# Optimization experiments

Hardware: AMD Instinct MI355X
Metric: run time of the kernel (lower is better)

## Reference

```python
import jax, jax.numpy as jnp
import numpy as np

N_ROUTING = 3


def squash(s):
    # squash factor ||s|| / (1 + ||s||^2), applied per output capsule vector
    n = jnp.linalg.norm(s, axis=-1, keepdims=True)
    return n / (1.0 + n * n) * s


def setup_inputs() -> dict:
    key = jax.random.key(0)
    k1, k2 = jax.random.split(key)
    B, Ni, Di = 64, 2048, 8
    No, Do = 32, 16
    x = jax.random.normal(k1, (B, Ni, Di), dtype=jnp.float32)
    W = jax.random.normal(k2, (Ni, No, Do, Di), dtype=jnp.float32) * 0.05
    return {"x": x, "W": W}


def reference(x, W):
    # x: (B, Ni, Di); W: (Ni, No, Do, Di)
    # Per-capsule transform: x_hat[b,i,j,:] = W[i,j] @ x[b,i]
    x_hat = jnp.einsum('bni,nodi->bnod', x, W)          # (B, Ni, No, Do)
    x_hat_sg = jax.lax.stop_gradient(x_hat)
    B, Ni, No, Do = x_hat.shape
    b = jnp.zeros((B, Ni, No), dtype=x_hat.dtype)       # routing logits
    v = None
    for it in range(N_ROUTING):
        c = jax.nn.softmax(b, axis=2)                   # coupling over output caps
        if it == N_ROUTING - 1:
            s = jnp.einsum('bno,bnod->bod', c, x_hat)   # grads flow on last iter
            v = squash(s)
        else:
            s = jnp.einsum('bno,bnod->bod', c, x_hat_sg)
            v = squash(s)
            b = b + jnp.einsum('bod,bnod->bno', v, x_hat_sg)  # agreement update
    return v  # (B, No, Do)
```

## Files before the change

### kernel.cpp

```cpp
#include <hip/hip_runtime.h>
#include <hip/hip_bf16.h>
#include <math.h>

namespace {
constexpr int kB  = 64;
constexpr int kNi = 2048;
constexpr int kNo = 32;
constexpr int kDo = 16;
constexpr int kSeg   = kNo * kDo;
constexpr int kSlabs = 256;
constexpr int kNPer  = kNi / kSlabs;
}

typedef __attribute__((ext_vector_type(4)))  short s4;
typedef __attribute__((ext_vector_type(16))) float f16v;

__device__ __forceinline__ f16v mfma_32x32x8_bf16(s4 a, s4 b, f16v c) {
#if __has_builtin(__builtin_amdgcn_mfma_f32_32x32x8bf16_1k)
    return __builtin_amdgcn_mfma_f32_32x32x8bf16_1k(a, b, c, 0, 0, 0);
#else
    asm("v_mfma_f32_32x32x8_bf16 %0, %1, %2, %0" : "+v"(c) : "v"(a), "v"(b));
    return c;
#endif
}

__device__ __forceinline__ unsigned pack_bf16(float lo, float hi) {
    union { __hip_bfloat162 h; unsigned u; } v;
    v.h = __float22bfloat162_rn(make_float2(lo, hi));
    return v.u;
}
__device__ __forceinline__ float bf_lo(unsigned u) { return __uint_as_float(u << 16); }
__device__ __forceinline__ float bf_hi(unsigned u) { return __uint_as_float(u & 0xffff0000u); }

union A2 { int2 i; s4 s; };

__global__ __launch_bounds__(256, 4)
void caps_prep(const float* __restrict__ xg, const float* __restrict__ Wg,
               unsigned* __restrict__ wPack2, unsigned* __restrict__ xPack)
{
    const int t = blockIdx.x * 256 + threadIdx.x;
    const int nW = kNi * 16 * 64;
    if (t < nW) {
        const int n = t >> 10, rem = t & 1023, mt = rem >> 6, l = rem & 63;
        const float4 w = *reinterpret_cast<const float4*>(
            Wg + ((size_t)n * kSeg + mt * 32 + (l & 31)) * 8 + 4 * (l >> 5));
        const size_t base = (((size_t)n * 8 + (mt >> 1)) * 64 + l) * 4 + (mt & 1) * 2;
        uint2 u; u.x = pack_bf16(w.x, w.y); u.y = pack_bf16(w.z, w.w);
        *reinterpret_cast<uint2*>(wPack2 + base) = u;
    } else {
        const int t2 = t - nW;
        const int n = t2 >> 7, rem = t2 & 127, nt = rem >> 6, l = rem & 63;
        const float4 v = *reinterpret_cast<const float4*>(
            xg + ((size_t)(nt * 32 + (l & 31)) * kNi + n) * 8 + 4 * (l >> 5));
        uint2 u; u.x = pack_bf16(v.x, v.y); u.y = pack_bf16(v.z, v.w);
        *reinterpret_cast<uint2*>(xPack + (size_t)t2 * 2) = u;
    }
}


__global__ __launch_bounds__(512, 2)
void caps_acc0(const unsigned* __restrict__ wPack2, const unsigned* __restrict__ xPack,
               __hip_bfloat16* __restrict__ partial)
{
    const int tid = threadIdx.x;
    const int blk = blockIdx.x & (kSlabs - 1);
    const int nt  = blockIdx.x >> 8;
    const int w   = __builtin_amdgcn_readfirstlane(tid >> 6);
    const int l   = tid & 63;
    const int b   = nt * 32 + (l & 31);
    const int hi  = l >> 5;

    f16v acc0, acc1;
#pragma unroll
    for (int r = 0; r < 16; ++r) { acc0[r] = 0.0f; acc1[r] = 0.0f; }

    const int4* wp4 = reinterpret_cast<const int4*>(wPack2);
    const int2* xp2 = reinterpret_cast<const int2*>(xPack);
    const size_t abase = ((size_t)blk * 64 + w) * 64 + l;
    const size_t xbase = ((size_t)blk * 16 + nt) * 64 + l;

#pragma unroll 2
    for (int nn = 0; nn < kNPer; ++nn) {
        const int4 aw = wp4[abase + (size_t)nn * 512];
        const int2 bx = xp2[xbase + (size_t)nn * 128];
        A2 ua0; ua0.i = make_int2(aw.x, aw.y);
        A2 ua1; ua1.i = make_int2(aw.z, aw.w);
        A2 ub;  ub.i  = bx;
        acc0 = mfma_32x32x8_bf16(ua0.s, ub.s, acc0);
        acc1 = mfma_32x32x8_bf16(ua1.s, ub.s, acc1);
    }

#pragma unroll
    for (int m = 0; m < 2; ++m) {
        const int mt = 2 * w + m;
        const f16v& a = (m == 0) ? acc0 : acc1;
#pragma unroll
        for (int q = 0; q < 4; ++q) {
            const int od = mt * 32 + 8 * q + 4 * hi;
            uint2 u;
            u.x = pack_bf16(a[4 * q + 0], a[4 * q + 1]);
            u.y = pack_bf16(a[4 * q + 2], a[4 * q + 3]);
            *reinterpret_cast<uint2*>(
                partial + ((size_t)blk * kB + b) * kSeg + od) = u;
        }
    }
}

__global__ __launch_bounds__(512, 2)
void caps_routef(const unsigned* __restrict__ wPack2, const unsigned* __restrict__ xPack,
                 const float* __restrict__ vsumPack, __hip_bfloat16* __restrict__ partial)
{
    __shared__ float Zl[2][8][4][32];
    __shared__ unsigned cl[kNPer][16][32];

    const int tid = threadIdx.x;
    const int blk = blockIdx.x & (kSlabs - 1);
    const int nt  = blockIdx.x >> 8;
    const int w   = __builtin_amdgcn_readfirstlane(tid >> 6);
    const int l   = tid & 63;
    const int b32 = l & 31;
    const int b   = nt * 32 + b32;
    const int hi  = l >> 5;

    const int4* wp4 = reinterpret_cast<const int4*>(wPack2);
    const int2* xp2 = reinterpret_cast<const int2*>(xPack);
    const size_t abase = ((size_t)blk * 64 + w) * 64 + l;
    const size_t xbase = ((size_t)blk * 16 + nt) * 64 + l;

    {
        float vsp[2][16];
#pragma unroll
        for (int m = 0; m < 2; ++m) {
            const int mt = 2 * w + m;
            const float4* vp = reinterpret_cast<const float4*>(
                vsumPack + (((size_t)mt * 2 + hi) * 64 + b) * 16);
#pragma unroll
            for (int k = 0; k < 4; ++k) {
                const float4 v = vp[k];
                vsp[m][4 * k + 0] = v.x; vsp[m][4 * k + 1] = v.y;
                vsp[m][4 * k + 2] = v.z; vsp[m][4 * k + 3] = v.w;
            }
        }

        for (int h = 0; h < 2; ++h) {
            float e[4][4];
#pragma unroll
            for (int k = 0; k < 4; ++k) {
                const int nn = h * 4 + k;
                const int4 aw = wp4[abase + (size_t)nn * 512];
                const int2 bx = xp2[xbase + (size_t)nn * 128];
                A2 ua0; ua0.i = make_int2(aw.x, aw.y);
                A2 ua1; ua1.i = make_int2(aw.z, aw.w);
                A2 ub;  ub.i  = bx;
                f16v t0, t1;
#pragma unroll
                for (int r = 0; r < 16; ++r) { t0[r] = 0.0f; t1[r] = 0.0f; }
                t0 = mfma_32x32x8_bf16(ua0.s, ub.s, t0);
                t1 = mfma_32x32x8_bf16(ua1.s, ub.s, t1);
                {
                    float a0_ = fmaf(vsp[0][1], t0[1], vsp[0][0] * t0[0]);
                    float a1_ = fmaf(vsp[0][3], t0[3], vsp[0][2] * t0[2]);
                    float a2_ = fmaf(vsp[0][5], t0[5], vsp[0][4] * t0[4]);
                    float a3_ = fmaf(vsp[0][7], t0[7], vsp[0][6] * t0[6]);
                    float p0 = (a0_ + a1_) + (a2_ + a3_);
                    float b0_ = fmaf(vsp[0][9],  t0[9],  vsp[0][8]  * t0[8]);
                    float b1_ = fmaf(vsp[0][11], t0[11], vsp[0][10] * t0[10]);
                    float b2_ = fmaf(vsp[0][13], t0[13], vsp[0][12] * t0[12]);
                    float b3_ = fmaf(vsp[0][15], t0[15], vsp[0][14] * t0[14]);
                    float p1 = (b0_ + b1_) + (b2_ + b3_);
                    p0 += __shfl_xor(p0, 32);
                    p1 += __shfl_xor(p1, 32);
                    e[k][0] = exp2f(p0); e[k][1] = exp2f(p1);
                }
                {
                    float a0_ = fmaf(vsp[1][1], t1[1], vsp[1][0] * t1[0]);
                    float a1_ = fmaf(vsp[1][3], t1[3], vsp[1][2] * t1[2]);
                    float a2_ = fmaf(vsp[1][5], t1[5], vsp[1][4] * t1[4]);
                    float a3_ = fmaf(vsp[1][7], t1[7], vsp[1][6] * t1[6]);
                    float p0 = (a0_ + a1_) + (a2_ + a3_);
                    float b0_ = fmaf(vsp[1][9],  t1[9],  vsp[1][8]  * t1[8]);
                    float b1_ = fmaf(vsp[1][11], t1[11], vsp[1][10] * t1[10]);
                    float b2_ = fmaf(vsp[1][13], t1[13], vsp[1][12] * t1[12]);
                    float b3_ = fmaf(vsp[1][15], t1[15], vsp[1][14] * t1[14]);
                    float p1 = (b0_ + b1_) + (b2_ + b3_);
                    p0 += __shfl_xor(p0, 32);
                    p1 += __shfl_xor(p1, 32);
                    e[k][2] = exp2f(p0); e[k][3] = exp2f(p1);
                }
                if (l < 32)
                    Zl[h][w][k][l] = (e[k][0] + e[k][1]) + (e[k][2] + e[k][3]);
            }
            __syncthreads();
#pragma unroll
            for (int k = 0; k < 4; ++k) {
                float Z = 0.0f;
#pragma unroll
                for (int w2 = 0; w2 < 8; ++w2) Z += Zl[h][w2][k][b32];
                const float rz = __builtin_amdgcn_rcpf(Z);
                if (l < 32) {
                    cl[h * 4 + k][2 * w + 0][l] = pack_bf16(e[k][0] * rz, e[k][1] * rz);
                    cl[h * 4 + k][2 * w + 1][l] = pack_bf16(e[k][2] * rz, e[k][3] * rz);
                }
            }
        }
    }
    __syncthreads();
    __builtin_amdgcn_sched_barrier(0);

    float sacc[2][16];
#pragma unroll
    for (int r = 0; r < 16; ++r) { sacc[0][r] = 0.0f; sacc[1][r] = 0.0f; }

#pragma unroll 2
    for (int nn = 0; nn < kNPer; ++nn) {
        const int4 aw = wp4[abase + (size_t)nn * 512];
        const int2 bx = xp2[xbase + (size_t)nn * 128];
        A2 ua0; ua0.i = make_int2(aw.x, aw.y);
        A2 ua1; ua1.i = make_int2(aw.z, aw.w);
        A2 ub;  ub.i  = bx;
        const unsigned cp0 = cl[nn][2 * w + 0][b32];
        const unsigned cp1 = cl[nn][2 * w + 1][b32];
        f16v t0, t1;
#pragma unroll
        for (int r = 0; r < 16; ++r) { t0[r] = 0.0f; t1[r] = 0.0f; }
        t0 = mfma_32x32x8_bf16(ua0.s, ub.s, t0);
        t1 = mfma_32x32x8_bf16(ua1.s, ub.s, t1);
        const float c00 = bf_lo(cp0), c01 = bf_hi(cp0);
        const float c10 = bf_lo(cp1), c11 = bf_hi(cp1);
#pragma unroll
        for (int r = 0; r < 8; ++r) {
            sacc[0][r]     = fmaf(c00, t0[r],     sacc[0][r]);
            sacc[0][8 + r] = fmaf(c01, t0[8 + r], sacc[0][8 + r]);
            sacc[1][r]     = fmaf(c10, t1[r],     sacc[1][r]);
            sacc[1][8 + r] = fmaf(c11, t1[8 + r], sacc[1][8 + r]);
        }
    }

#pragma unroll
    for (int m = 0; m < 2; ++m) {
        const int mt = 2 * w + m;
#pragma unroll
        for (int q = 0; q < 4; ++q) {
            const int od = mt * 32 + 8 * q + 4 * hi;
            uint2 u;
            u.x = pack_bf16(sacc[m][4 * q + 0], sacc[m][4 * q + 1]);
            u.y = pack_bf16(sacc[m][4 * q + 2], sacc[m][4 * q + 3]);
            *reinterpret_cast<uint2*>(
                partial + ((size_t)blk * kB + b) * kSeg + od) = u;
        }
    }
}

template<int PASS>
__global__ __launch_bounds__(512, 2)
void caps_finish(const __hip_bfloat16* __restrict__ partial,
                 float* __restrict__ vsum, float* __restrict__ vsumPack,
                 float* __restrict__ out)
{
    const int b  = blockIdx.x >> 2;
    const int q  = blockIdx.x & 3;
    const int t  = threadIdx.x;
    const int tl = t & 127;
    const int cg = t >> 7;
    const int od = q * 128 + tl;

    const __hip_bfloat16* p = partial
        + ((size_t)(cg * 64) * kB + b) * kSeg + od;
    float s = 0.0f;
#pragma unroll 16
    for (int k = 0; k < 64; ++k)
        s += __bfloat162float(p[(size_t)k * (kB * kSeg)]);

    __shared__ float red[4][128];
    __shared__ float sq[128];
    __shared__ float fo[8];
    red[cg][tl] = s;
    __syncthreads();
    if (t < 128) {
        s = (red[0][tl] + red[1][tl]) + (red[2][tl] + red[3][tl]);
        if (PASS == 0) s *= (1.0f / 32.0f);
        sq[tl] = s * s;
    }
    __syncthreads();
    if (t < 8) {
        float n2 = 0.0f;
#pragma unroll
        for (int d = 0; d < 16; ++d) n2 += sq[t * 16 + d];
        fo[t] = sqrtf(n2) / (1.0f + n2);
    }
    __syncthreads();
    if (t < 128) {
        const float v = fo[tl >> 4] * s;
        float nv = v;
        if (PASS == 0) {
            vsum[(size_t)b * kSeg + od] = v;
        } else if (PASS == 1) {
            nv = vsum[(size_t)b * kSeg + od] + v;
            vsum[(size_t)b * kSeg + od] = nv;
        } else {
            out[(size_t)b * kSeg + od] = v;
        }
        if (PASS < 2) {
            const int mt = od >> 5, r5 = od & 31;
            const int hi = (r5 >> 2) & 1, reg = (r5 & 3) | ((r5 >> 3) << 2);
            vsumPack[(((size_t)mt * 2 + hi) * 64 + b) * 16 + reg] =
                nv * 1.44269504f;
        }
    }
}

extern "C" void kernel_launch(void* const* d_in, const int* in_sizes, int n_in,
                              void* d_out, int out_size, void* d_ws, size_t ws_size,
                              hipStream_t stream)
{
    const float* x = (const float*)d_in[0];
    const float* W = (const float*)d_in[1];
    float* out = (float*)d_out;

    char* base = (char*)d_ws;
    __hip_bfloat16* partial = (__hip_bfloat16*)base;
    base += (size_t)kSlabs * kB * kSeg * sizeof(__hip_bfloat16);
    float* vsum = (float*)base;
    base += (size_t)kB * kSeg * sizeof(float);
    float* vsumPack = (float*)base;
    base += (size_t)16 * 2 * 64 * 16 * sizeof(float);
    unsigned* wPack2 = (unsigned*)base;
    base += (size_t)kNi * 16 * 64 * 2 * sizeof(unsigned);
    unsigned* xPack = (unsigned*)base;

    caps_prep<<<dim3(9216), dim3(256), 0, stream>>>(x, W, wPack2, xPack);

    const dim3 gr(kSlabs * 2), br(512);
    const dim3 gf(kB * 4), bf(512);

    caps_acc0<<<gr, br, 0, stream>>>(wPack2, xPack, partial);
    caps_finish<0><<<gf, bf, 0, stream>>>(partial, vsum, vsumPack, out);
    caps_routef<<<gr, br, 0, stream>>>(wPack2, xPack, vsumPack, partial);
    caps_finish<1><<<gf, bf, 0, stream>>>(partial, vsum, vsumPack, out);
    caps_routef<<<gr, br, 0, stream>>>(wPack2, xPack, vsumPack, partial);
    caps_finish<2><<<gf, bf, 0, stream>>>(partial, vsum, vsumPack, out);
}
```

Before: 79.41 us.

## Fuse bf16 packing into first accumulation pass and vectorize finish reduction

The separate prep kernel is removed. The first routing accumulation kernel now reads fp32 W and x directly, packs them to bf16 and writes the packed buffers for later passes while also consuming them for its MFMA accumulation. Each block now covers both batch tiles, which halves the grid to 256 blocks, and each W load feeds four MFMAs. The finish kernel reads four bf16 values per load over 16 slab groups and reduces them through a larger shared array. This saves one launch and a round trip of the packed data, at the cost of fewer blocks in the fused kernel and more per-thread work.

```diff
diff --git a/kernel.cpp b/kernel.cpp
--- a/kernel.cpp
+++ b/kernel.cpp
@@ -34,74 +34,75 @@
 
 union A2 { int2 i; s4 s; };
 
-__global__ __launch_bounds__(256, 4)
-void caps_prep(const float* __restrict__ xg, const float* __restrict__ Wg,
-               unsigned* __restrict__ wPack2, unsigned* __restrict__ xPack)
-{
-    const int t = blockIdx.x * 256 + threadIdx.x;
-    const int nW = kNi * 16 * 64;
-    if (t < nW) {
-        const int n = t >> 10, rem = t & 1023, mt = rem >> 6, l = rem & 63;
-        const float4 w = *reinterpret_cast<const float4*>(
-            Wg + ((size_t)n * kSeg + mt * 32 + (l & 31)) * 8 + 4 * (l >> 5));
-        const size_t base = (((size_t)n * 8 + (mt >> 1)) * 64 + l) * 4 + (mt & 1) * 2;
-        uint2 u; u.x = pack_bf16(w.x, w.y); u.y = pack_bf16(w.z, w.w);
-        *reinterpret_cast<uint2*>(wPack2 + base) = u;
-    } else {
-        const int t2 = t - nW;
-        const int n = t2 >> 7, rem = t2 & 127, nt = rem >> 6, l = rem & 63;
-        const float4 v = *reinterpret_cast<const float4*>(
-            xg + ((size_t)(nt * 32 + (l & 31)) * kNi + n) * 8 + 4 * (l >> 5));
-        uint2 u; u.x = pack_bf16(v.x, v.y); u.y = pack_bf16(v.z, v.w);
-        *reinterpret_cast<uint2*>(xPack + (size_t)t2 * 2) = u;
-    }
-}
-
 
 __global__ __launch_bounds__(512, 2)
-void caps_acc0(const unsigned* __restrict__ wPack2, const unsigned* __restrict__ xPack,
-               __hip_bfloat16* __restrict__ partial)
+void caps_prepacc(const float* __restrict__ xg, const float* __restrict__ Wg,
+                  unsigned* __restrict__ wPack2, unsigned* __restrict__ xPack,
+                  __hip_bfloat16* __restrict__ partial)
 {
     const int tid = threadIdx.x;
-    const int blk = blockIdx.x & (kSlabs - 1);
-    const int nt  = blockIdx.x >> 8;
+    const int blk = blockIdx.x;
     const int w   = __builtin_amdgcn_readfirstlane(tid >> 6);
     const int l   = tid & 63;
-    const int b   = nt * 32 + (l & 31);
+    const int o32 = l & 31;
     const int hi  = l >> 5;
 
-    f16v acc0, acc1;
-#pragma unroll
-    for (int r = 0; r < 16; ++r) { acc0[r] = 0.0f; acc1[r] = 0.0f; }
-
-    const int4* wp4 = reinterpret_cast<const int4*>(wPack2);
-    const int2* xp2 = reinterpret_cast<const int2*>(xPack);
-    const size_t abase = ((size_t)blk * 64 + w) * 64 + l;
-    const size_t xbase = ((size_t)blk * 16 + nt) * 64 + l;
+    const float4* Wg4 = reinterpret_cast<const float4*>(Wg);
+    const float4* xg4 = reinterpret_cast<const float4*>(xg);
+
+    f16v acc00, acc01, acc10, acc11;
+#pragma unroll
+    for (int r = 0; r < 16; ++r) {
+        acc00[r] = 0.0f; acc01[r] = 0.0f; acc10[r] = 0.0f; acc11[r] = 0.0f;
+    }
 
 #pragma unroll 2
     for (int nn = 0; nn < kNPer; ++nn) {
-        const int4 aw = wp4[abase + (size_t)nn * 512];
-        const int2 bx = xp2[xbase + (size_t)nn * 128];
-        A2 ua0; ua0.i = make_int2(aw.x, aw.y);
-        A2 ua1; ua1.i = make_int2(aw.z, aw.w);
-        A2 ub;  ub.i  = bx;
-        acc0 = mfma_32x32x8_bf16(ua0.s, ub.s, acc0);
-        acc1 = mfma_32x32x8_bf16(ua1.s, ub.s, acc1);
-    }
-
-#pragma unroll
-    for (int m = 0; m < 2; ++m) {
-        const int mt = 2 * w + m;
-        const f16v& a = (m == 0) ? acc0 : acc1;
-#pragma unroll
-        for (int q = 0; q < 4; ++q) {
-            const int od = mt * 32 + 8 * q + 4 * hi;
-            uint2 u;
-            u.x = pack_bf16(a[4 * q + 0], a[4 * q + 1]);
-            u.y = pack_bf16(a[4 * q + 2], a[4 * q + 3]);
-            *reinterpret_cast<uint2*>(
-                partial + ((size_t)blk * kB + b) * kSeg + od) = u;
+        const int n = blk * kNPer + nn;
+        const float4 w0 = Wg4[((size_t)n * 512 + (2 * w + 0) * 32 + o32) * 2 + hi];
+        const float4 w1 = Wg4[((size_t)n * 512 + (2 * w + 1) * 32 + o32) * 2 + hi];
+        int4 wp;
+        wp.x = (int)pack_bf16(w0.x, w0.y);
+        wp.y = (int)pack_bf16(w0.z, w0.w);
+        wp.z = (int)pack_bf16(w1.x, w1.y);
+        wp.w = (int)pack_bf16(w1.z, w1.w);
+        reinterpret_cast<int4*>(wPack2)[((size_t)n * 8 + w) * 64 + l] = wp;
+
+        const float4 x0 = xg4[((size_t)(0 * 32 + o32) * kNi + n) * 2 + hi];
+        const float4 x1 = xg4[((size_t)(32 + o32) * kNi + n) * 2 + hi];
+        uint2 q0, q1;
+        q0.x = pack_bf16(x0.x, x0.y); q0.y = pack_bf16(x0.z, x0.w);
+        q1.x = pack_bf16(x1.x, x1.y); q1.y = pack_bf16(x1.z, x1.w);
+        *reinterpret_cast<uint2*>(xPack + ((size_t)(n * 2 + 0) * 64 + l) * 2) = q0;
+        *reinterpret_cast<uint2*>(xPack + ((size_t)(n * 2 + 1) * 64 + l) * 2) = q1;
+
+        A2 a0; a0.i = make_int2(wp.x, wp.y);
+        A2 a1; a1.i = make_int2(wp.z, wp.w);
+        A2 b0; b0.i = make_int2((int)q0.x, (int)q0.y);
+        A2 b1; b1.i = make_int2((int)q1.x, (int)q1.y);
+        acc00 = mfma_32x32x8_bf16(a0.s, b0.s, acc00);
+        acc01 = mfma_32x32x8_bf16(a1.s, b0.s, acc01);
+        acc10 = mfma_32x32x8_bf16(a0.s, b1.s, acc10);
+        acc11 = mfma_32x32x8_bf16(a1.s, b1.s, acc11);
+    }
+
+#pragma unroll
+    for (int nt = 0; nt < 2; ++nt) {
+        const int b = nt * 32 + o32;
+#pragma unroll
+        for (int m = 0; m < 2; ++m) {
+            const int mt = 2 * w + m;
+            const f16v& a = (nt == 0) ? (m == 0 ? acc00 : acc01)
+                                      : (m == 0 ? acc10 : acc11);
+#pragma unroll
+            for (int q = 0; q < 4; ++q) {
+                const int od = mt * 32 + 8 * q + 4 * hi;
+                uint2 u;
+                u.x = pack_bf16(a[4 * q + 0], a[4 * q + 1]);
+                u.y = pack_bf16(a[4 * q + 2], a[4 * q + 3]);
+                *reinterpret_cast<uint2*>(
+                    partial + ((size_t)blk * kB + b) * kSeg + od) = u;
+            }
         }
     }
 }
@@ -260,26 +261,32 @@
     const int b  = blockIdx.x >> 2;
     const int q  = blockIdx.x & 3;
     const int t  = threadIdx.x;
-    const int tl = t & 127;
-    const int cg = t >> 7;
-    const int od = q * 128 + tl;
+    const int qd = t & 31;
+    const int sg = t >> 5;
+    const int od0 = q * 128 + qd * 4;
 
     const __hip_bfloat16* p = partial
-        + ((size_t)(cg * 64) * kB + b) * kSeg + od;
-    float s = 0.0f;
-#pragma unroll 16
-    for (int k = 0; k < 64; ++k)
-        s += __bfloat162float(p[(size_t)k * (kB * kSeg)]);
-
-    __shared__ float red[4][128];
+        + ((size_t)(sg * 16) * kB + b) * kSeg + od0;
+    float s0 = 0, s1 = 0, s2 = 0, s3 = 0;
+#pragma unroll
+    for (int k = 0; k < 16; ++k) {
+        const uint2 u = *reinterpret_cast<const uint2*>(p + (size_t)k * (kB * kSeg));
+        s0 += bf_lo(u.x); s1 += bf_hi(u.x);
+        s2 += bf_lo(u.y); s3 += bf_hi(u.y);
+    }
+
+    __shared__ float red[16][128];
     __shared__ float sq[128];
     __shared__ float fo[8];
-    red[cg][tl] = s;
+    *reinterpret_cast<float4*>(&red[sg][qd * 4]) = make_float4(s0, s1, s2, s3);
     __syncthreads();
     if (t < 128) {
-        s = (red[0][tl] + red[1][tl]) + (red[2][tl] + red[3][tl]);
+        float s = 0.0f;
+#pragma unroll
+        for (int g = 0; g < 16; ++g) s += red[g][t];
         if (PASS == 0) s *= (1.0f / 32.0f);
-        sq[tl] = s * s;
+        sq[t] = s * s;
+        red[0][t] = s;
     }
     __syncthreads();
     if (t < 8) {
@@ -290,7 +297,9 @@
     }
     __syncthreads();
     if (t < 128) {
-        const float v = fo[tl >> 4] * s;
+        const float s = red[0][t];
+        const int od = q * 128 + t;
+        const float v = fo[t >> 4] * s;
         float nv = v;
         if (PASS == 0) {
             vsum[(size_t)b * kSeg + od] = v;
@@ -328,12 +337,11 @@
     base += (size_t)kNi * 16 * 64 * 2 * sizeof(unsigned);
     unsigned* xPack = (unsigned*)base;
 
-    caps_prep<<<dim3(9216), dim3(256), 0, stream>>>(x, W, wPack2, xPack);
-
+    const dim3 gp(kSlabs), bp(512);
     const dim3 gr(kSlabs * 2), br(512);
     const dim3 gf(kB * 4), bf(512);
 
-    caps_acc0<<<gr, br, 0, stream>>>(wPack2, xPack, partial);
+    caps_prepacc<<<gp, bp, 0, stream>>>(x, W, wPack2, xPack, partial);
     caps_finish<0><<<gf, bf, 0, stream>>>(partial, vsum, vsumPack, out);
     caps_routef<<<gr, br, 0, stream>>>(wPack2, xPack, vsumPack, partial);
     caps_finish<1><<<gf, bf, 0, stream>>>(partial, vsum, vsumPack, out);
```

New measurement: 71.87 us. 9.5% less time.
